# Optimization experiments

Hardware: AMD Instinct MI355X
Metric: run time of the kernel (lower is better)

## Reference

```python
import jax, jax.numpy as jnp
import numpy as np

E = 1024; H = 16; D = E // H; T = 1024; B = 4; L = 8; R = 4


def setup_inputs() -> dict:
    key = jax.random.key(0)
    ks = jax.random.split(key, 24)
    std = float(np.sqrt(2.0 / (E + E)))
    n = lambda i, shape, s: (jax.random.normal(ks[i], shape, jnp.float32) * s)
    inp = {
        'input': jax.random.normal(ks[0], (T, B, E), jnp.float32),
        'pos': jax.random.normal(ks[1], (T, 1, E), jnp.float32),
        'indices': jax.random.randint(ks[2], (1,), 0, L),
        'in_proj_weight': n(3, (3 * E, E), std),
        'in_proj_bias': jnp.zeros((3 * E,), jnp.float32),
        'out_proj_weight': n(4, (E, E), std),
        'out_proj_bias': jnp.zeros((E,), jnp.float32),
        'pos_proj_weight': n(5, (E, E), std),
        'pos_proj_bias': jnp.zeros((E,), jnp.float32),
        'r_i': n(6, (L, R, 3 * E), 0.02), 's_i': n(7, (L, R, E), 0.02),
        'r_p': n(8, (L, R, E), 0.02), 's_p': n(9, (L, R, E), 0.02),
        'r_o': n(10, (L, R, E), 0.02), 's_o': n(11, (L, R, E), 0.02),
        'rm_i': 1.0 + n(12, (L, 1, 3 * E), 0.02), 'sm_i': 1.0 + n(13, (L, 1, E), 0.02),
        'rm_p': 1.0 + n(14, (L, 1, E), 0.02), 'sm_p': 1.0 + n(15, (L, 1, E), 0.02),
        'rm_o': 1.0 + n(16, (L, 1, E), 0.02), 'sm_o': 1.0 + n(17, (L, 1, E), 0.02),
        'r_w_bias': n(18, (H, D), 0.02),
        'r_r_bias': n(19, (H, D), 0.02),
    }
    return inp


def _rel_shift(x):
    # Transformer-XL relative shift. x: [B, H, q, k]
    b, h, q, k = x.shape
    x = jnp.pad(x, ((0, 0), (0, 0), (0, 0), (1, 0)))
    return x.reshape(b, h, k + 1, q)[:, :, 1:, :].reshape(b, h, q, k)


def _factorize(W, rm, sm, r, s):
    # multiplicative: W * sum_k outer(rm_k, sm_k); additive low-rank: + sum_k outer(r_k, s_k)
    W = W * jnp.einsum('ka,kb->ab', rm, sm)
    return W + jnp.einsum('ka,kb->ab', r, s)


def reference(input, pos, indices, in_proj_weight, in_proj_bias, out_proj_weight,
              out_proj_bias, pos_proj_weight, pos_proj_bias, r_i, s_i, r_p, s_p,
              r_o, s_o, rm_i, sm_i, rm_p, sm_p, rm_o, sm_o, r_w_bias, r_r_bias):
    idx = indices[0]
    tk = lambda p: jnp.take(p, idx, axis=0)
    Wi = _factorize(in_proj_weight, tk(rm_i), tk(sm_i), tk(r_i), tk(s_i))
    Wo = _factorize(out_proj_weight, tk(rm_o), tk(sm_o), tk(r_o), tk(s_o))
    Wp = _factorize(pos_proj_weight, tk(rm_p), tk(sm_p), tk(r_p), tk(s_p))

    t, b, e = input.shape
    qkv = input @ Wi.T + in_proj_bias            # [T, B, 3E]
    q, k, v = jnp.split(qkv, 3, axis=-1)
    q = q.reshape(t, b, H, D)
    k = k.reshape(t, b, H, D)
    v = v.reshape(t, b, H, D)
    r = (pos[:, 0] @ Wp.T + pos_proj_bias).reshape(-1, H, D)  # [S, H, D]

    scale = 1.0 / np.sqrt(D)
    AC = jnp.einsum('tbhd,sbhd->bhts', q + r_w_bias, k)       # content score
    BD = _rel_shift(jnp.einsum('tbhd,shd->bhts', q + r_r_bias, r))  # position score
    attn = jax.nn.softmax((AC + BD) * scale, axis=-1)
    out = jnp.einsum('bhts,sbhd->tbhd', attn, v).reshape(t, b, e)
    return out @ Wo.T + out_proj_bias
```

## Files before the change

### kernel.cpp

```cpp
#include <hip/hip_runtime.h>
#include <hip/hip_bf16.h>
#include <math.h>

#define E_DIM  1024
#define H_DIM  16
#define D_DIM  64
#define T_SEQ  1024
#define B_SZ   4
#define E3     3072
#define R_RANK 4

typedef __attribute__((ext_vector_type(8))) short bf16x8;
typedef __attribute__((ext_vector_type(8))) unsigned short u16x8;
typedef __attribute__((ext_vector_type(4))) float f32x4;

static __device__ __forceinline__ ushort f2bf(float x) {
  __hip_bfloat16 h = __float2bfloat16(x);
  return *(ushort*)&h;
}
static __device__ __forceinline__ float bf2f(ushort u) {
  unsigned int v = ((unsigned int)u) << 16;
  float f;
  __builtin_memcpy(&f, &v, 4);
  return f;
}

static __device__ __forceinline__ void barrier_lgkm() {
  asm volatile("s_waitcnt lgkmcnt(0)" ::: "memory");
  __builtin_amdgcn_s_barrier();
  __builtin_amdgcn_sched_barrier(0);
}

#define GLOAD_LDS16(g, l)                                                     \
  __builtin_amdgcn_global_load_lds(                                           \
      (const __attribute__((address_space(1))) void*)(g),                     \
      (__attribute__((address_space(3))) void*)(l), 16, 0, 0)

static __device__ __forceinline__ void fact4(
    const float* __restrict__ W, const float* __restrict__ rm,
    const float* __restrict__ sm, const float* __restrict__ r,
    const float* __restrict__ s, ushort* __restrict__ out,
    int A, int idx, long long t) {
  long long i4 = t * 4;
  int a = (int)(i4 >> 10);
  int bcol = (int)(i4 & 1023);
  float4 wv = *(const float4*)(W + i4);
  float ra = rm[(long long)idx * A + a];
  float4 sv = *(const float4*)(sm + (long long)idx * 1024 + bcol);
  float4 acc;
  acc.x = wv.x * ra * sv.x; acc.y = wv.y * ra * sv.y;
  acc.z = wv.z * ra * sv.z; acc.w = wv.w * ra * sv.w;
#pragma unroll
  for (int k = 0; k < R_RANK; ++k) {
    float rk = r[((long long)idx * R_RANK + k) * A + a];
    float4 sk = *(const float4*)(s + ((long long)idx * R_RANK + k) * 1024 + bcol);
    acc.x += rk * sk.x; acc.y += rk * sk.y;
    acc.z += rk * sk.z; acc.w += rk * sk.w;
  }
  ushort4 o;
  o.x = f2bf(acc.x); o.y = f2bf(acc.y); o.z = f2bf(acc.z); o.w = f2bf(acc.w);
  *(ushort4*)(out + i4) = o;
}

__global__ __launch_bounds__(256) void prep_kernel(
    const float* __restrict__ input, const float* __restrict__ pos,
    const float* __restrict__ in_w, const float* __restrict__ pos_w,
    const float* __restrict__ out_w,
    const float* __restrict__ rm_i, const float* __restrict__ sm_i,
    const float* __restrict__ r_i, const float* __restrict__ s_i,
    const float* __restrict__ rm_p, const float* __restrict__ sm_p,
    const float* __restrict__ r_p, const float* __restrict__ s_p,
    const float* __restrict__ rm_o, const float* __restrict__ sm_o,
    const float* __restrict__ r_o, const float* __restrict__ s_o,
    const int* __restrict__ idxp,
    ushort* __restrict__ ibf, ushort* __restrict__ pbf,
    ushort* __restrict__ Wi, ushort* __restrict__ Wp,
    ushort* __restrict__ Wo) {
  const int idx = idxp[0];
  long long t = (long long)blockIdx.x * blockDim.x + threadIdx.x;
  if (t < 524288) {
    float4 v0 = *(const float4*)(input + t * 8);
    float4 v1 = *(const float4*)(input + t * 8 + 4);
    ushort4 o0, o1;
    o0.x = f2bf(v0.x); o0.y = f2bf(v0.y); o0.z = f2bf(v0.z); o0.w = f2bf(v0.w);
    o1.x = f2bf(v1.x); o1.y = f2bf(v1.y); o1.z = f2bf(v1.z); o1.w = f2bf(v1.w);
    *(ushort4*)(ibf + t * 8) = o0;
    *(ushort4*)(ibf + t * 8 + 4) = o1;
    return;
  }
  t -= 524288;
  if (t < 131072) {
    float4 v0 = *(const float4*)(pos + t * 8);
    float4 v1 = *(const float4*)(pos + t * 8 + 4);
    ushort4 o0, o1;
    o0.x = f2bf(v0.x); o0.y = f2bf(v0.y); o0.z = f2bf(v0.z); o0.w = f2bf(v0.w);
    o1.x = f2bf(v1.x); o1.y = f2bf(v1.y); o1.z = f2bf(v1.z); o1.w = f2bf(v1.w);
    *(ushort4*)(pbf + t * 8) = o0;
    *(ushort4*)(pbf + t * 8 + 4) = o1;
    return;
  }
  t -= 131072;
  if (t < 786432) { fact4(in_w, rm_i, sm_i, r_i, s_i, Wi, E3, idx, t); return; }
  t -= 786432;
  if (t < 262144) { fact4(pos_w, rm_p, sm_p, r_p, s_p, Wp, E_DIM, idx, t); return; }
  t -= 262144;
  fact4(out_w, rm_o, sm_o, r_o, s_o, Wo, E_DIM, idx, t);
}

template <bool BF16OUT>
static __device__ __forceinline__ void gemm_body(
    const ushort* __restrict__ A, const ushort* __restrict__ B,
    const float* __restrict__ bias, void* __restrict__ Cv,
    int N, int K, int m0, int n0, ushort* As, ushort* Bs) {
  const int tid = threadIdx.x;
  const int l = tid & 63, w = tid >> 6;
  const int mw = (w >> 1) * 64, nw = (w & 1) * 64;
  const int fr = l & 15, fq = l >> 4;
  const int lrow = l >> 2;
  const int lk = (l & 3) * 8;

  f32x4 acc[4][4];
#pragma unroll
  for (int i = 0; i < 4; ++i)
#pragma unroll
    for (int j = 0; j < 4; ++j)
#pragma unroll
      for (int q = 0; q < 4; ++q) acc[i][j][q] = 0.f;

  for (int k0 = 0; k0 < K; k0 += 32) {
    __syncthreads();
#pragma unroll
    for (int p = 0; p < 2; ++p) {
      int row = w * 32 + p * 16;
      GLOAD_LDS16(A + (long long)(m0 + row + lrow) * K + k0 + lk,
                  As + row * 32);
      GLOAD_LDS16(B + (long long)(n0 + row + lrow) * K + k0 + lk,
                  Bs + row * 32);
    }
    __syncthreads();
    bf16x8 af[4], bfr[4];
#pragma unroll
    for (int i = 0; i < 4; ++i) {
      af[i]  = *(const bf16x8*)(As + (mw + i * 16 + fr) * 32 + fq * 8);
      bfr[i] = *(const bf16x8*)(Bs + (nw + i * 16 + fr) * 32 + fq * 8);
    }
#pragma unroll
    for (int i = 0; i < 4; ++i)
#pragma unroll
      for (int j = 0; j < 4; ++j)
        acc[i][j] = __builtin_amdgcn_mfma_f32_16x16x32_bf16(
            af[i], bfr[j], acc[i][j], 0, 0, 0);
  }
#pragma unroll
  for (int i = 0; i < 4; ++i) {
#pragma unroll
    for (int j = 0; j < 4; ++j) {
      int n = n0 + nw + j * 16 + fr;
      float bv = bias[n];
#pragma unroll
      for (int q = 0; q < 4; ++q) {
        int m = m0 + mw + i * 16 + fq * 4 + q;
        if constexpr (BF16OUT)
          ((ushort*)Cv)[(long long)m * N + n] = f2bf(acc[i][j][q] + bv);
        else
          ((float*)Cv)[(long long)m * N + n] = acc[i][j][q] + bv;
      }
    }
  }
}

__global__ __launch_bounds__(256) void gemm_qkvpos_kernel(
    const ushort* __restrict__ ibf, const ushort* __restrict__ Wi,
    const float* __restrict__ in_b, ushort* __restrict__ qkvb,
    const ushort* __restrict__ pbf, const ushort* __restrict__ Wp,
    const float* __restrict__ pos_b, ushort* __restrict__ rbufb) {
  __shared__ __align__(16) ushort As[128 * 32];
  __shared__ __align__(16) ushort Bs[128 * 32];
  int f = blockIdx.x;
  if (f < 768) {
    gemm_body<true>(ibf, Wi, in_b, qkvb, E3, E_DIM,
                    (f / 24) * 128, (f % 24) * 128, As, Bs);
  } else {
    int f2 = f - 768;
    gemm_body<true>(pbf, Wp, pos_b, rbufb, E_DIM, E_DIM,
                    (f2 / 8) * 128, (f2 % 8) * 128, As, Bs);
  }
}

__global__ __launch_bounds__(256) void gemm_out_kernel(
    const ushort* __restrict__ A, const ushort* __restrict__ B,
    const float* __restrict__ bias, float* __restrict__ C,
    int M, int N, int K) {
  __shared__ __align__(16) ushort As[128 * 32];
  __shared__ __align__(16) ushort Bs[128 * 32];
  gemm_body<false>(A, B, bias, C, N, K,
                   blockIdx.y * 128, blockIdx.x * 128, As, Bs);
}

static __device__ __forceinline__ int kri(int row, int d) {
  return (row * 72 + d) ^ ((row & 8) ? 8 : 0);
}
static __device__ __forceinline__ int vdi(int d, int s) {
  return 64 * 72 + ((d * 72 + s) ^ (((d >> 3) & 7) << 3));
}

__global__ __launch_bounds__(256) void attn12_kernel(
    const ushort* __restrict__ qkv, const ushort* __restrict__ rb,
    const float* __restrict__ rwb, const float* __restrict__ rrb,
    ushort* __restrict__ outb) {
  __shared__ __align__(16) ushort Xls[128 * 72];
  __shared__ __align__(16) ushort Q4ls[16 * 72];
  __shared__ __align__(16) ushort Wb[65 * 136];

  const int flat = blockIdx.y * 16 + blockIdx.x;
  const int swz = (flat & 7) * 128 + (flat >> 3);
  const int t0 = (swz & 15) * 64;
  const int byy = swz >> 4;
  const int b = byy >> 4, h = byy & 15;

  const int tid = threadIdx.x;
  const int l = tid & 63, w = tid >> 6;
  const int fr = l & 15, fq = l >> 4;
  const int srow = tid >> 2;
  const int sd0 = (tid & 3) * 16;

  {
    long long qo = ((long long)(t0 + srow) * B_SZ + b) * E3 + h * 64 + sd0;
#pragma unroll
    for (int j = 0; j < 16; ++j)
      Xls[kri(srow, sd0 + j)] =
          f2bf(bf2f(qkv[qo + j]) + rwb[h * 64 + sd0 + j]);
  }
  __syncthreads();
  const bf16x8 bQw0 = *(const bf16x8*)(Xls + kri(16 * w + fr, fq * 8));
  const bf16x8 bQw1 = *(const bf16x8*)(Xls + kri(16 * w + fr, fq * 8 + 32));
  __syncthreads();
  {
    long long qo = ((long long)(t0 + srow) * B_SZ + b) * E3 + h * 64 + sd0;
#pragma unroll
    for (int j = 0; j < 16; ++j)
      Xls[kri(srow, sd0 + j)] =
          f2bf(bf2f(qkv[qo + j]) + rrb[h * 64 + sd0 + j]);
  }
  if (tid < 64) {
    int row = tid >> 2;
    int d0 = (tid & 3) * 16;
    if (row == 0 && t0 + 64 < T_SEQ) {
      long long qo = ((long long)(t0 + 64) * B_SZ + b) * E3 + h * 64 + d0;
#pragma unroll
      for (int j = 0; j < 16; ++j)
        Q4ls[kri(row, d0 + j)] =
            f2bf(bf2f(qkv[qo + j]) + rrb[h * 64 + d0 + j]);
    } else {
#pragma unroll
      for (int j = 0; j < 16; ++j) Q4ls[kri(row, d0 + j)] = 0;
    }
  }
  __syncthreads();
  bf16x8 bQr0[4], bQr1[4];
#pragma unroll
  for (int j = 0; j < 4; ++j) {
    bQr0[j] = *(const bf16x8*)(Xls + kri(16 * j + fr, fq * 8));
    bQr1[j] = *(const bf16x8*)(Xls + kri(16 * j + fr, fq * 8 + 32));
  }
  __syncthreads();

  auto wphase = [&](int rbase, int rowbase) {
    bf16x8 a0 = *(const bf16x8*)(Xls + kri(rowbase + 16 * w + fr, fq * 8));
    bf16x8 a1 = *(const bf16x8*)(Xls + kri(rowbase + 16 * w + fr, fq * 8 + 32));
    const int cb = (rbase & 64) + 16 * w + 4 * fq;
#pragma unroll
    for (int j = 0; j < 4; ++j) {
      f32x4 acw;
#pragma unroll
      for (int q = 0; q < 4; ++q) acw[q] = 0.f;
      acw = __builtin_amdgcn_mfma_f32_16x16x32_bf16(a0, bQr0[j], acw, 0, 0, 0);
      acw = __builtin_amdgcn_mfma_f32_16x16x32_bf16(a1, bQr1[j], acw, 0, 0, 0);
      ushort4 pk;
      pk.x = f2bf(acw[0]); pk.y = f2bf(acw[1]);
      pk.z = f2bf(acw[2]); pk.w = f2bf(acw[3]);
      *(ushort4*)(Wb + (16 * j + fr) * 136 + cb) = pk;
      if (cb == 0)
        *(ushort4*)(Wb + (16 * j + fr) * 136 + 128) = pk;
    }
    {
      bf16x8 q40 = *(const bf16x8*)(Q4ls + kri(fr, fq * 8));
      bf16x8 q41 = *(const bf16x8*)(Q4ls + kri(fr, fq * 8 + 32));
      f32x4 acw;
#pragma unroll
      for (int q = 0; q < 4; ++q) acw[q] = 0.f;
      acw = __builtin_amdgcn_mfma_f32_16x16x32_bf16(a0, q40, acw, 0, 0, 0);
      acw = __builtin_amdgcn_mfma_f32_16x16x32_bf16(a1, q41, acw, 0, 0, 0);
      if (fr == 0) {
        ushort4 pk;
        pk.x = f2bf(acw[0]); pk.y = f2bf(acw[1]);
        pk.z = f2bf(acw[2]); pk.w = f2bf(acw[3]);
        *(ushort4*)(Wb + 64 * 136 + cb) = pk;
        if (cb == 0) *(ushort4*)(Wb + 64 * 136 + 128) = pk;
      }
    }
  };

  u16x8 kr0, kr1, rr0, rr1;
  auto loadK = [&](int ti) {
    long long ko =
        ((long long)(ti * 64 + srow) * B_SZ + b) * E3 + E_DIM + h * 64 + sd0;
    kr0 = *(const u16x8*)(qkv + ko);
    kr1 = *(const u16x8*)(qkv + ko + 8);
  };
  auto loadR = [&](int ti) {
    int g = 1024 + 64 * ti - t0 + srow;
    int cr = (g <= 1023) ? g : g - 1025;
#pragma unroll
    for (int j = 0; j < 8; ++j) { rr0[j] = 0; rr1[j] = 0; }
    if (cr >= 0 && cr < 1024) {
      long long ro = (long long)cr * E_DIM + h * 64 + sd0;
      rr0 = *(const u16x8*)(rb + ro);
      rr1 = *(const u16x8*)(rb + ro + 8);
    }
  };

  {
    int g = 960 - t0 + srow;
    u16x8 r0, r1;
#pragma unroll
    for (int j = 0; j < 8; ++j) { r0[j] = 0; r1[j] = 0; }
    if (g >= 0) {
      long long ro = (long long)g * E_DIM + h * 64 + sd0;
      r0 = *(const u16x8*)(rb + ro);
      r1 = *(const u16x8*)(rb + ro + 8);
    }
    *(u16x8*)(Xls + kri(64 + srow, sd0)) = r0;
    *(u16x8*)(Xls + kri(64 + srow, sd0 + 8)) = r1;
  }
  loadK(0);
  loadR(0);
  barrier_lgkm();
  wphase(0, 64);
  barrier_lgkm();

  float m_s = -1e30f, l_s = 0.f;
  f32x4 oacc[4];
#pragma unroll
  for (int c = 0; c < 4; ++c)
#pragma unroll
    for (int q = 0; q < 4; ++q) oacc[c][q] = 0.f;

  const int dt_ = 16 * w + fr;
  const int diag = t0 >> 6;
  const ushort* rowp = Wb + dt_ * 136;
  int cb4[4];
#pragma unroll
  for (int i = 0; i < 4; ++i)
    cb4[i] = (63 + 16 * i + 4 * fq - dt_) & 127;

  for (int ti = 0; ti < 16; ++ti) {
    const int s0 = ti * 64;
    *(u16x8*)(Xls + kri(srow, sd0)) = kr0;
    *(u16x8*)(Xls + kri(srow, sd0 + 8)) = kr1;
    *(u16x8*)(Xls + kri(64 + srow, sd0)) = rr0;
    *(u16x8*)(Xls + kri(64 + srow, sd0 + 8)) = rr1;
    if (ti < 15) {
      loadK(ti + 1);
      loadR(ti + 1);
    }
    u16x8 v0, v1;
    {
      long long vo =
          ((long long)(s0 + srow) * B_SZ + b) * E3 + 2 * E_DIM + h * 64 + sd0;
      v0 = *(const u16x8*)(qkv + vo);
      v1 = *(const u16x8*)(qkv + vo + 8);
    }
    barrier_lgkm();

    __builtin_amdgcn_s_setprio(1);
    f32x4 accS[4];
#pragma unroll
    for (int c = 0; c < 4; ++c)
#pragma unroll
      for (int q = 0; q < 4; ++q) accS[c][q] = 0.f;
#pragma unroll
    for (int i = 0; i < 4; ++i) {
      bf16x8 a0 = *(const bf16x8*)(Xls + kri(16 * i + fr, fq * 8));
      bf16x8 a1 = *(const bf16x8*)(Xls + kri(16 * i + fr, fq * 8 + 32));
      accS[i] = __builtin_amdgcn_mfma_f32_16x16x32_bf16(a0, bQw0, accS[i], 0, 0, 0);
      accS[i] = __builtin_amdgcn_mfma_f32_16x16x32_bf16(a1, bQw1, accS[i], 0, 0, 0);
    }
    wphase(64 * (ti + 1), 64);
    __builtin_amdgcn_s_setprio(0);
    barrier_lgkm();

    float pmax = -1e30f;
    if (ti != diag) {
#pragma unroll
      for (int i = 0; i < 4; ++i) {
        const ushort* rp = rowp + cb4[i];
#pragma unroll
        for (int q = 0; q < 4; ++q) {
          float sc = (accS[i][q] + bf2f(rp[q])) * 0.125f;
          accS[i][q] = sc;
          pmax = fmaxf(pmax, sc);
        }
      }
    } else {
      const int thr = t0 - s0;
      const int cadd = 64 * ti + 63;
#pragma unroll
      for (int i = 0; i < 4; ++i) {
#pragma unroll
        for (int q = 0; q < 4; ++q) {
          const int delta = 16 * i + 4 * fq + q - dt_;
          const int sel = (delta > thr) ? 1 : 0;
          const int c = (cadd + delta) & 127;
          float Wv = (delta == thr + 1) ? 0.f : bf2f(Wb[(dt_ + sel) * 136 + c]);
          float sc = (accS[i][q] + Wv) * 0.125f;
          accS[i][q] = sc;
          pmax = fmaxf(pmax, sc);
        }
      }
    }
#pragma unroll
    for (int i = 0; i < 4; ++i) cb4[i] ^= 64;
    if (ti == diag) rowp += 136;

    pmax = fmaxf(pmax, __shfl_xor(pmax, 16));
    pmax = fmaxf(pmax, __shfl_xor(pmax, 32));
    float mnew = fmaxf(m_s, pmax);
    float alpha = __expf(m_s - mnew);
    m_s = mnew;
    float ps = 0.f;
#pragma unroll
    for (int i = 0; i < 4; ++i) {
      ushort4 pk;
      float p0 = __expf(accS[i][0] - mnew);
      float p1 = __expf(accS[i][1] - mnew);
      float p2 = __expf(accS[i][2] - mnew);
      float p3 = __expf(accS[i][3] - mnew);
      ps += p0 + p1 + p2 + p3;
      pk.x = f2bf(p0); pk.y = f2bf(p1); pk.z = f2bf(p2); pk.w = f2bf(p3);
      *(ushort4*)(Xls + kri(dt_, 16 * i + 4 * fq)) = pk;
    }
    ps += __shfl_xor(ps, 16);
    ps += __shfl_xor(ps, 32);
    l_s = l_s * alpha + ps;
    float av[4];
#pragma unroll
    for (int q = 0; q < 4; ++q) av[q] = __shfl(alpha, 4 * fq + q);
#pragma unroll
    for (int cfd = 0; cfd < 4; ++cfd)
#pragma unroll
      for (int q = 0; q < 4; ++q) oacc[cfd][q] *= av[q];
#pragma unroll
    for (int j = 0; j < 8; ++j) {
      Xls[vdi(sd0 + j, srow)] = (ushort)v0[j];
      Xls[vdi(sd0 + 8 + j, srow)] = (ushort)v1[j];
    }
    barrier_lgkm();

    __builtin_amdgcn_s_setprio(1);
#pragma unroll
    for (int ks = 0; ks < 2; ++ks) {
      bf16x8 aP = *(const bf16x8*)(Xls + kri(16 * w + fr, fq * 8 + 32 * ks));
#pragma unroll
      for (int cfd = 0; cfd < 4; ++cfd) {
        bf16x8 bV = *(const bf16x8*)(Xls + vdi(16 * cfd + fr, fq * 8 + 32 * ks));
        oacc[cfd] =
            __builtin_amdgcn_mfma_f32_16x16x32_bf16(aP, bV, oacc[cfd], 0, 0, 0);
      }
    }
    __builtin_amdgcn_s_setprio(0);
    barrier_lgkm();
  }

  float linv[4];
#pragma unroll
  for (int q = 0; q < 4; ++q) linv[q] = 1.f / __shfl(l_s, 4 * fq + q);
#pragma unroll
  for (int q = 0; q < 4; ++q) {
    int t = t0 + 16 * w + 4 * fq + q;
#pragma unroll
    for (int cfd = 0; cfd < 4; ++cfd)
      outb[((long long)t * B_SZ + b) * E_DIM + h * 64 + 16 * cfd + fr] =
          f2bf(oacc[cfd][q] * linv[q]);
  }
}

extern "C" void kernel_launch(void* const* d_in, const int* in_sizes, int n_in,
                              void* d_out, int out_size, void* d_ws,
                              size_t ws_size, hipStream_t stream) {
  const float* input = (const float*)d_in[0];
  const float* pos   = (const float*)d_in[1];
  const int*   idx   = (const int*)d_in[2];
  const float* in_w  = (const float*)d_in[3];
  const float* in_b  = (const float*)d_in[4];
  const float* out_w = (const float*)d_in[5];
  const float* out_b = (const float*)d_in[6];
  const float* pos_w = (const float*)d_in[7];
  const float* pos_b = (const float*)d_in[8];
  const float* r_i   = (const float*)d_in[9];
  const float* s_i   = (const float*)d_in[10];
  const float* r_p   = (const float*)d_in[11];
  const float* s_p   = (const float*)d_in[12];
  const float* r_o   = (const float*)d_in[13];
  const float* s_o   = (const float*)d_in[14];
  const float* rm_i  = (const float*)d_in[15];
  const float* sm_i  = (const float*)d_in[16];
  const float* rm_p  = (const float*)d_in[17];
  const float* sm_p  = (const float*)d_in[18];
  const float* rm_o  = (const float*)d_in[19];
  const float* sm_o  = (const float*)d_in[20];
  const float* rwb   = (const float*)d_in[21];
  const float* rrb   = (const float*)d_in[22];
  float* out = (float*)d_out;

  char* base = (char*)d_ws;
  ushort* qkvb  = (ushort*)(base);
  ushort* rbufb = (ushort*)(base + 24ll * 1024 * 1024);
  ushort* Wi    = (ushort*)(base + 26ll * 1024 * 1024);
  ushort* Wp    = (ushort*)(base + 32ll * 1024 * 1024);
  ushort* Wo    = (ushort*)(base + 34ll * 1024 * 1024);
  ushort* ibf   = (ushort*)(base + 36ll * 1024 * 1024);
  ushort* pbf   = (ushort*)(base + 44ll * 1024 * 1024);
  ushort* abf   = ibf;

  prep_kernel<<<7680, 256, 0, stream>>>(
      input, pos, in_w, pos_w, out_w,
      rm_i, sm_i, r_i, s_i, rm_p, sm_p, r_p, s_p, rm_o, sm_o, r_o, s_o,
      idx, ibf, pbf, Wi, Wp, Wo);
  gemm_qkvpos_kernel<<<832, 256, 0, stream>>>(
      ibf, Wi, in_b, qkvb, pbf, Wp, pos_b, rbufb);
  attn12_kernel<<<dim3(16, 64), 256, 0, stream>>>(
      qkvb, rbufb, rwb, rrb, abf);
  gemm_out_kernel<<<dim3(E_DIM / 128, (T_SEQ * B_SZ) / 128), 256, 0, stream>>>(
      abf, Wo, out_b, out, T_SEQ * B_SZ, E_DIM, E_DIM);
}
```

Measured before the change: 192.2 us.

## Double-buffer K/R shared tiles in attention kernel and prefetch two tiles ahead

The attention kernel now keeps two LDS buffers for the K and R tiles. The next tile is written into the alternate buffer while the current one is consumed, which removes one barrier per iteration. Global loads of K and R are issued two iterations ahead, and the Q4 fragments are hoisted into registers. The cost is about double the LDS footprint, which may lower occupancy, and more live registers.

Result: slower. 242.7 us (+26.3%).

```diff
diff --git a/kernel.cpp b/kernel.cpp
--- a/kernel.cpp
+++ b/kernel.cpp
@@ -204,11 +204,11 @@
   return 64 * 72 + ((d * 72 + s) ^ (((d >> 3) & 7) << 3));
 }
 
-__global__ __launch_bounds__(256) void attn12_kernel(
+__global__ __launch_bounds__(256) void attn13_kernel(
     const ushort* __restrict__ qkv, const ushort* __restrict__ rb,
     const float* __restrict__ rwb, const float* __restrict__ rrb,
     ushort* __restrict__ outb) {
-  __shared__ __align__(16) ushort Xls[128 * 72];
+  __shared__ __align__(16) ushort Xls2[2][128 * 72];
   __shared__ __align__(16) ushort Q4ls[16 * 72];
   __shared__ __align__(16) ushort Wb[65 * 136];
 
@@ -224,82 +224,8 @@
   const int srow = tid >> 2;
   const int sd0 = (tid & 3) * 16;
 
-  {
-    long long qo = ((long long)(t0 + srow) * B_SZ + b) * E3 + h * 64 + sd0;
-#pragma unroll
-    for (int j = 0; j < 16; ++j)
-      Xls[kri(srow, sd0 + j)] =
-          f2bf(bf2f(qkv[qo + j]) + rwb[h * 64 + sd0 + j]);
-  }
-  __syncthreads();
-  const bf16x8 bQw0 = *(const bf16x8*)(Xls + kri(16 * w + fr, fq * 8));
-  const bf16x8 bQw1 = *(const bf16x8*)(Xls + kri(16 * w + fr, fq * 8 + 32));
-  __syncthreads();
-  {
-    long long qo = ((long long)(t0 + srow) * B_SZ + b) * E3 + h * 64 + sd0;
-#pragma unroll
-    for (int j = 0; j < 16; ++j)
-      Xls[kri(srow, sd0 + j)] =
-          f2bf(bf2f(qkv[qo + j]) + rrb[h * 64 + sd0 + j]);
-  }
-  if (tid < 64) {
-    int row = tid >> 2;
-    int d0 = (tid & 3) * 16;
-    if (row == 0 && t0 + 64 < T_SEQ) {
-      long long qo = ((long long)(t0 + 64) * B_SZ + b) * E3 + h * 64 + d0;
-#pragma unroll
-      for (int j = 0; j < 16; ++j)
-        Q4ls[kri(row, d0 + j)] =
-            f2bf(bf2f(qkv[qo + j]) + rrb[h * 64 + d0 + j]);
-    } else {
-#pragma unroll
-      for (int j = 0; j < 16; ++j) Q4ls[kri(row, d0 + j)] = 0;
-    }
-  }
-  __syncthreads();
-  bf16x8 bQr0[4], bQr1[4];
-#pragma unroll
-  for (int j = 0; j < 4; ++j) {
-    bQr0[j] = *(const bf16x8*)(Xls + kri(16 * j + fr, fq * 8));
-    bQr1[j] = *(const bf16x8*)(Xls + kri(16 * j + fr, fq * 8 + 32));
-  }
-  __syncthreads();
-
-  auto wphase = [&](int rbase, int rowbase) {
-    bf16x8 a0 = *(const bf16x8*)(Xls + kri(rowbase + 16 * w + fr, fq * 8));
-    bf16x8 a1 = *(const bf16x8*)(Xls + kri(rowbase + 16 * w + fr, fq * 8 + 32));
-    const int cb = (rbase & 64) + 16 * w + 4 * fq;
-#pragma unroll
-    for (int j = 0; j < 4; ++j) {
-      f32x4 acw;
-#pragma unroll
-      for (int q = 0; q < 4; ++q) acw[q] = 0.f;
-      acw = __builtin_amdgcn_mfma_f32_16x16x32_bf16(a0, bQr0[j], acw, 0, 0, 0);
-      acw = __builtin_amdgcn_mfma_f32_16x16x32_bf16(a1, bQr1[j], acw, 0, 0, 0);
-      ushort4 pk;
-      pk.x = f2bf(acw[0]); pk.y = f2bf(acw[1]);
-      pk.z = f2bf(acw[2]); pk.w = f2bf(acw[3]);
-      *(ushort4*)(Wb + (16 * j + fr) * 136 + cb) = pk;
-      if (cb == 0)
-        *(ushort4*)(Wb + (16 * j + fr) * 136 + 128) = pk;
-    }
-    {
-      bf16x8 q40 = *(const bf16x8*)(Q4ls + kri(fr, fq * 8));
-      bf16x8 q41 = *(const bf16x8*)(Q4ls + kri(fr, fq * 8 + 32));
-      f32x4 acw;
-#pragma unroll
-      for (int q = 0; q < 4; ++q) acw[q] = 0.f;
-      acw = __builtin_amdgcn_mfma_f32_16x16x32_bf16(a0, q40, acw, 0, 0, 0);
-      acw = __builtin_amdgcn_mfma_f32_16x16x32_bf16(a1, q41, acw, 0, 0, 0);
-      if (fr == 0) {
-        ushort4 pk;
-        pk.x = f2bf(acw[0]); pk.y = f2bf(acw[1]);
-        pk.z = f2bf(acw[2]); pk.w = f2bf(acw[3]);
-        *(ushort4*)(Wb + 64 * 136 + cb) = pk;
-        if (cb == 0) *(ushort4*)(Wb + 64 * 136 + 128) = pk;
-      }
-    }
-  };
+  ushort* X0 = Xls2[0];
+  ushort* X1 = Xls2[1];
 
   u16x8 kr0, kr1, rr0, rr1;
   auto loadK = [&](int ti) {
@@ -319,7 +245,41 @@
       rr1 = *(const u16x8*)(rb + ro + 8);
     }
   };
-
+  loadK(0);
+  loadR(0);
+
+  {
+    long long qo = ((long long)(t0 + srow) * B_SZ + b) * E3 + h * 64 + sd0;
+#pragma unroll
+    for (int j = 0; j < 16; ++j)
+      X0[kri(srow, sd0 + j)] =
+          f2bf(bf2f(qkv[qo + j]) + rwb[h * 64 + sd0 + j]);
+  }
+  __syncthreads();
+  const bf16x8 bQw0 = *(const bf16x8*)(X0 + kri(16 * w + fr, fq * 8));
+  const bf16x8 bQw1 = *(const bf16x8*)(X0 + kri(16 * w + fr, fq * 8 + 32));
+  __syncthreads();
+  {
+    long long qo = ((long long)(t0 + srow) * B_SZ + b) * E3 + h * 64 + sd0;
+#pragma unroll
+    for (int j = 0; j < 16; ++j)
+      X0[kri(srow, sd0 + j)] =
+          f2bf(bf2f(qkv[qo + j]) + rrb[h * 64 + sd0 + j]);
+  }
+  if (tid < 64) {
+    int row = tid >> 2;
+    int d0 = (tid & 3) * 16;
+    if (row == 0 && t0 + 64 < T_SEQ) {
+      long long qo = ((long long)(t0 + 64) * B_SZ + b) * E3 + h * 64 + d0;
+#pragma unroll
+      for (int j = 0; j < 16; ++j)
+        Q4ls[kri(row, d0 + j)] =
+            f2bf(bf2f(qkv[qo + j]) + rrb[h * 64 + d0 + j]);
+    } else {
+#pragma unroll
+      for (int j = 0; j < 16; ++j) Q4ls[kri(row, d0 + j)] = 0;
+    }
+  }
   {
     int g = 960 - t0 + srow;
     u16x8 r0, r1;
@@ -330,13 +290,61 @@
       r0 = *(const u16x8*)(rb + ro);
       r1 = *(const u16x8*)(rb + ro + 8);
     }
-    *(u16x8*)(Xls + kri(64 + srow, sd0)) = r0;
-    *(u16x8*)(Xls + kri(64 + srow, sd0 + 8)) = r1;
-  }
-  loadK(0);
-  loadR(0);
-  barrier_lgkm();
-  wphase(0, 64);
+    *(u16x8*)(X1 + kri(64 + srow, sd0)) = r0;
+    *(u16x8*)(X1 + kri(64 + srow, sd0 + 8)) = r1;
+  }
+  __syncthreads();
+  bf16x8 bQr0[4], bQr1[4];
+#pragma unroll
+  for (int j = 0; j < 4; ++j) {
+    bQr0[j] = *(const bf16x8*)(X0 + kri(16 * j + fr, fq * 8));
+    bQr1[j] = *(const bf16x8*)(X0 + kri(16 * j + fr, fq * 8 + 32));
+  }
+  const bf16x8 bQ40 = *(const bf16x8*)(Q4ls + kri(fr, fq * 8));
+  const bf16x8 bQ41 = *(const bf16x8*)(Q4ls + kri(fr, fq * 8 + 32));
+  __syncthreads();
+
+  auto wphase = [&](int rbase, const ushort* Xbuf) {
+    bf16x8 a0 = *(const bf16x8*)(Xbuf + kri(64 + 16 * w + fr, fq * 8));
+    bf16x8 a1 = *(const bf16x8*)(Xbuf + kri(64 + 16 * w + fr, fq * 8 + 32));
+    const int cb = (rbase & 64) + 16 * w + 4 * fq;
+#pragma unroll
+    for (int j = 0; j < 4; ++j) {
+      f32x4 acw;
+#pragma unroll
+      for (int q = 0; q < 4; ++q) acw[q] = 0.f;
+      acw = __builtin_amdgcn_mfma_f32_16x16x32_bf16(a0, bQr0[j], acw, 0, 0, 0);
+      acw = __builtin_amdgcn_mfma_f32_16x16x32_bf16(a1, bQr1[j], acw, 0, 0, 0);
+      ushort4 pk;
+      pk.x = f2bf(acw[0]); pk.y = f2bf(acw[1]);
+      pk.z = f2bf(acw[2]); pk.w = f2bf(acw[3]);
+      *(ushort4*)(Wb + (16 * j + fr) * 136 + cb) = pk;
+      if (cb == 0)
+        *(ushort4*)(Wb + (16 * j + fr) * 136 + 128) = pk;
+    }
+    {
+      f32x4 acw;
+#pragma unroll
+      for (int q = 0; q < 4; ++q) acw[q] = 0.f;
+      acw = __builtin_amdgcn_mfma_f32_16x16x32_bf16(a0, bQ40, acw, 0, 0, 0);
+      acw = __builtin_amdgcn_mfma_f32_16x16x32_bf16(a1, bQ41, acw, 0, 0, 0);
+      if (fr == 0) {
+        ushort4 pk;
+        pk.x = f2bf(acw[0]); pk.y = f2bf(acw[1]);
+        pk.z = f2bf(acw[2]); pk.w = f2bf(acw[3]);
+        *(ushort4*)(Wb + 64 * 136 + cb) = pk;
+        if (cb == 0) *(ushort4*)(Wb + 64 * 136 + 128) = pk;
+      }
+    }
+  };
+
+  wphase(0, X1);
+  *(u16x8*)(X0 + kri(srow, sd0)) = kr0;
+  *(u16x8*)(X0 + kri(srow, sd0 + 8)) = kr1;
+  *(u16x8*)(X0 + kri(64 + srow, sd0)) = rr0;
+  *(u16x8*)(X0 + kri(64 + srow, sd0 + 8)) = rr1;
+  loadK(1);
+  loadR(1);
   barrier_lgkm();
 
   float m_s = -1e30f, l_s = 0.f;
@@ -356,13 +364,18 @@
 
   for (int ti = 0; ti < 16; ++ti) {
     const int s0 = ti * 64;
-    *(u16x8*)(Xls + kri(srow, sd0)) = kr0;
-    *(u16x8*)(Xls + kri(srow, sd0 + 8)) = kr1;
-    *(u16x8*)(Xls + kri(64 + srow, sd0)) = rr0;
-    *(u16x8*)(Xls + kri(64 + srow, sd0 + 8)) = rr1;
+    const int p = ti & 1;
+    ushort* Xp = Xls2[p];
+    ushort* Xq = Xls2[p ^ 1];
     if (ti < 15) {
-      loadK(ti + 1);
-      loadR(ti + 1);
+      *(u16x8*)(Xq + kri(srow, sd0)) = kr0;
+      *(u16x8*)(Xq + kri(srow, sd0 + 8)) = kr1;
+      *(u16x8*)(Xq + kri(64 + srow, sd0)) = rr0;
+      *(u16x8*)(Xq + kri(64 + srow, sd0 + 8)) = rr1;
+    }
+    if (ti < 14) {
+      loadK(ti + 2);
+      loadR(ti + 2);
     }
     u16x8 v0, v1;
     {
@@ -371,7 +384,6 @@
       v0 = *(const u16x8*)(qkv + vo);
       v1 = *(const u16x8*)(qkv + vo + 8);
     }
-    barrier_lgkm();
 
     __builtin_amdgcn_s_setprio(1);
     f32x4 accS[4];
@@ -381,12 +393,12 @@
       for (int q = 0; q < 4; ++q) accS[c][q] = 0.f;
 #pragma unroll
     for (int i = 0; i < 4; ++i) {
-      bf16x8 a0 = *(const bf16x8*)(Xls + kri(16 * i + fr, fq * 8));
-      bf16x8 a1 = *(const bf16x8*)(Xls + kri(16 * i + fr, fq * 8 + 32));
+      bf16x8 a0 = *(const bf16x8*)(Xp + kri(16 * i + fr, fq * 8));
+      bf16x8 a1 = *(const bf16x8*)(Xp + kri(16 * i + fr, fq * 8 + 32));
       accS[i] = __builtin_amdgcn_mfma_f32_16x16x32_bf16(a0, bQw0, accS[i], 0, 0, 0);
       accS[i] = __builtin_amdgcn_mfma_f32_16x16x32_bf16(a1, bQw1, accS[i], 0, 0, 0);
     }
-    wphase(64 * (ti + 1), 64);
+    wphase(64 * (ti + 1), Xp);
     __builtin_amdgcn_s_setprio(0);
     barrier_lgkm();
 
@@ -438,7 +450,7 @@
       float p3 = __expf(accS[i][3] - mnew);
       ps += p0 + p1 + p2 + p3;
       pk.x = f2bf(p0); pk.y = f2bf(p1); pk.z = f2bf(p2); pk.w = f2bf(p3);
-      *(ushort4*)(Xls + kri(dt_, 16 * i + 4 * fq)) = pk;
+      *(ushort4*)(Xp + kri(dt_, 16 * i + 4 * fq)) = pk;
     }
     ps += __shfl_xor(ps, 16);
     ps += __shfl_xor(ps, 32);
@@ -452,18 +464,18 @@
       for (int q = 0; q < 4; ++q) oacc[cfd][q] *= av[q];
 #pragma unroll
     for (int j = 0; j < 8; ++j) {
-      Xls[vdi(sd0 + j, srow)] = (ushort)v0[j];
-      Xls[vdi(sd0 + 8 + j, srow)] = (ushort)v1[j];
+      Xp[vdi(sd0 + j, srow)] = (ushort)v0[j];
+      Xp[vdi(sd0 + 8 + j, srow)] = (ushort)v1[j];
     }
     barrier_lgkm();
 
     __builtin_amdgcn_s_setprio(1);
 #pragma unroll
     for (int ks = 0; ks < 2; ++ks) {
-      bf16x8 aP = *(const bf16x8*)(Xls + kri(16 * w + fr, fq * 8 + 32 * ks));
+      bf16x8 aP = *(const bf16x8*)(Xp + kri(16 * w + fr, fq * 8 + 32 * ks));
 #pragma unroll
       for (int cfd = 0; cfd < 4; ++cfd) {
-        bf16x8 bV = *(const bf16x8*)(Xls + vdi(16 * cfd + fr, fq * 8 + 32 * ks));
+        bf16x8 bV = *(const bf16x8*)(Xp + vdi(16 * cfd + fr, fq * 8 + 32 * ks));
         oacc[cfd] =
             __builtin_amdgcn_mfma_f32_16x16x32_bf16(aP, bV, oacc[cfd], 0, 0, 0);
       }
@@ -529,7 +541,7 @@
       idx, ibf, pbf, Wi, Wp, Wo);
   gemm_qkvpos_kernel<<<832, 256, 0, stream>>>(
       ibf, Wi, in_b, qkvb, pbf, Wp, pos_b, rbufb);
-  attn12_kernel<<<dim3(16, 64), 256, 0, stream>>>(
+  attn13_kernel<<<dim3(16, 64), 256, 0, stream>>>(
       qkvb, rbufb, rwb, rrb, abf);
   gemm_out_kernel<<<dim3(E_DIM / 128, (T_SEQ * B_SZ) / 128), 256, 0, stream>>>(
       abf, Wo, out_b, out, T_SEQ * B_SZ, E_DIM, E_DIM);
```
